# Performance work log

Hardware: AMD Instinct MI355X
Metric: run time of the kernel (lower is better)

The kernel has to match this reference:

```python
import jax, jax.numpy as jnp
import numpy as np

B, M, IN, H = 4096, 16, 512, 512


def _linear_params(key, out_dim, in_dim):
    kw, kb = jax.random.split(key)
    s = 1.0 / np.sqrt(in_dim)
    W = jax.random.uniform(kw, (out_dim, in_dim), jnp.float32, -s, s)
    b = jax.random.uniform(kb, (out_dim,), jnp.float32, -s, s)
    return W, b


def setup_inputs() -> dict:
    key = jax.random.key(0)
    ks = jax.random.split(key, 15)
    inp = {
        "input": jax.random.normal(ks[0], (B, IN), jnp.float32),
        "h0": jax.random.normal(ks[1], (B, H), jnp.float32),
        "c0": jax.random.normal(ks[2], (B, H), jnp.float32),
        "all_c_b_e_w": jax.random.normal(ks[3], (B, M, H), jnp.float32),
        "all_num_word": jax.random.randint(ks[4], (B,), 0, M + 1, jnp.int32),
    }
    names = ["ii", "hi", "if_", "hf", "ig", "hg", "io", "ho", "lx", "lc"]
    in_dims = [IN, H, IN, H, IN, H, IN, H, IN, H]
    for n, d, k in zip(names, in_dims, ks[5:15]):
        W, b = _linear_params(k, H, d)
        inp["W_" + n] = W
        inp["b_" + n] = b
    return inp


def _lin(x, W, b):
    return x @ W.T + b


def reference(input, h0, c0, all_c_b_e_w, all_num_word,
              W_ii, b_ii, W_hi, b_hi, W_if_, b_if_, W_hf, b_hf,
              W_ig, b_ig, W_hg, b_hg, W_io, b_io, W_ho, b_ho,
              W_lx, b_lx, W_lc, b_lc):
    i = jax.nn.sigmoid(_lin(input, W_ii, b_ii) + _lin(h0, W_hi, b_hi))   # [B,H]
    f = jax.nn.sigmoid(_lin(input, W_if_, b_if_) + _lin(h0, W_hf, b_hf))  # computed but unused, as in original
    g = jnp.tanh(_lin(input, W_ig, b_ig) + _lin(h0, W_hg, b_hg))         # [B,H]
    o = jax.nn.sigmoid(_lin(input, W_io, b_io) + _lin(h0, W_ho, b_ho))   # [B,H]

    # lattice word-cell gates, vectorized over the ragged word dim with a mask
    lx = _lin(input, W_lx, b_lx)                 # [B,H]
    lc = _lin(all_c_b_e_w, W_lc, b_lc)           # [B,M,H]
    i_b = jax.nn.sigmoid(lx[:, None, :] + lc)    # [B,M,H]
    mask = (jnp.arange(M)[None, :] < all_num_word[:, None])  # [B,M]
    exp_b = jnp.exp(i_b) * mask[:, :, None].astype(i_b.dtype)  # [B,M,H]
    exp_i = jnp.exp(i)                                         # [B,H]
    denom = exp_i + jnp.sum(exp_b, axis=1)                     # [B,H]
    c_words = jnp.sum((exp_b / denom[:, None, :]) * all_c_b_e_w, axis=1)
    c_lat = c_words + (exp_i / denom) * g
    c = jnp.where((all_num_word > 0)[:, None], c_lat, g)       # num_word==0 -> c=g
    h1 = o * jnp.tanh(c)
    return (h1, c)
```

## Files before the change

kernel.cpp:

```cpp
#include <hip/hip_runtime.h>
#include <stdint.h>


typedef __attribute__((ext_vector_type(8))) short short8;
typedef __attribute__((ext_vector_type(4))) float f32x4;
typedef __attribute__((ext_vector_type(4))) unsigned short us4;

__device__ __forceinline__ unsigned short f2bf(float f) {
  union { float f; unsigned u; } v; v.f = f;
  return (unsigned short)((v.u + 0x7fffu + ((v.u >> 16) & 1u)) >> 16);
}
__device__ __forceinline__ float bf2f(unsigned short u) {
  return __uint_as_float((unsigned)u << 16);
}
__device__ __forceinline__ float sigmoidf_(float x) {
  return 1.f / (1.f + __expf(-x));
}
__device__ __forceinline__ float fast_tanh(float x) {
  float e = __expf(-2.f * fmaxf(x, -30.f));
  return (1.f - e) / (1.f + e);
}

__global__ void k_cvt_xh(const float* __restrict__ x, const float* __restrict__ h,
                         unsigned short* __restrict__ out) {
  int t = blockIdx.x * blockDim.x + threadIdx.x;
  int b = t >> 8;
  int col = (t & 255) * 4;
  const float* src = (col < 512) ? (x + (size_t)b * 512 + col)
                                 : (h + (size_t)b * 512 + (col - 512));
  f32x4 v = *(const f32x4*)src;
  us4 o;
  o[0] = f2bf(v[0]); o[1] = f2bf(v[1]); o[2] = f2bf(v[2]); o[3] = f2bf(v[3]);
  *(us4*)(out + (size_t)t * 4) = o;
}

__global__ void k_cvt_w(const float* __restrict__ Wii, const float* __restrict__ Wig,
                        const float* __restrict__ Wio, const float* __restrict__ Wlx,
                        const float* __restrict__ Whi, const float* __restrict__ Whg,
                        const float* __restrict__ Who, unsigned short* __restrict__ out) {
  int t = blockIdx.x * blockDim.x + threadIdx.x;
  int row = t >> 8;
  int col = (t & 255) * 4;
  int sec = row >> 9, r = row & 511;
  us4 o;
  if (col < 512) {
    const float* W = sec == 0 ? Wii : sec == 1 ? Wig : sec == 2 ? Wio : Wlx;
    f32x4 v = *(const f32x4*)(W + (size_t)r * 512 + col);
    o[0] = f2bf(v[0]); o[1] = f2bf(v[1]); o[2] = f2bf(v[2]); o[3] = f2bf(v[3]);
  } else if (sec < 3) {
    const float* W = sec == 0 ? Whi : sec == 1 ? Whg : Who;
    f32x4 v = *(const f32x4*)(W + (size_t)r * 512 + (col - 512));
    o[0] = f2bf(v[0]); o[1] = f2bf(v[1]); o[2] = f2bf(v[2]); o[3] = f2bf(v[3]);
  } else {
    o[0] = 0; o[1] = 0; o[2] = 0; o[3] = 0;
  }
  *(us4*)(out + (size_t)t * 4) = o;
}

__global__ void k_cvt_wlc(const float* __restrict__ src, unsigned short* __restrict__ out) {
  int t = blockIdx.x * blockDim.x + threadIdx.x;
  f32x4 v = *(const f32x4*)(src + (size_t)t * 4);
  us4 o;
  o[0] = f2bf(v[0]); o[1] = f2bf(v[1]); o[2] = f2bf(v[2]); o[3] = f2bf(v[3]);
  *(us4*)(out + (size_t)t * 4) = o;
}

__global__ __launch_bounds__(256) void k_gemm0(
    const unsigned short* __restrict__ A, const unsigned short* __restrict__ Bm,
    unsigned short* __restrict__ C, int Ndim, int Kdim, int nbx) {
  __shared__ unsigned short As[2][128 * 64];
  __shared__ unsigned short Bs[2][128 * 64];
  const int tid = threadIdx.x;
  const int lane = tid & 63, wid = tid >> 6;
  const int wr = wid >> 1, wc = wid & 1;
  const int l15 = lane & 15, lhi = lane >> 4;

  const int chunk = gridDim.x >> 3;
  const int bid = (blockIdx.x & 7) * chunk + (blockIdx.x >> 3);
  const int brow = bid / nbx, bcol = bid % nbx;
  const int m0 = brow * 128, n0 = bcol * 128;

  f32x4 acc[4][4];
#pragma unroll
  for (int i = 0; i < 4; ++i)
#pragma unroll
    for (int j = 0; j < 4; ++j) acc[i][j] = (f32x4){0.f, 0.f, 0.f, 0.f};

  const int cb0 = wid * 64;
  auto stage = [&](int buf, int k0) {
#pragma unroll
    for (int q = 0; q < 4; ++q) {
      const int cb = q * 256 + cb0;
      const int chunkid = cb + lane;
      const int row = chunkid >> 3, slot = chunkid & 7;
      const int kk = k0 + ((slot ^ (row & 7)) << 3);
      __builtin_amdgcn_global_load_lds(
          (const __attribute__((address_space(1))) unsigned int*)(A + (size_t)(m0 + row) * Kdim + kk),
          (__attribute__((address_space(3))) unsigned int*)(As[buf] + cb * 8), 16, 0, 0);
      __builtin_amdgcn_global_load_lds(
          (const __attribute__((address_space(1))) unsigned int*)(Bm + (size_t)(n0 + row) * Kdim + kk),
          (__attribute__((address_space(3))) unsigned int*)(Bs[buf] + cb * 8), 16, 0, 0);
    }
  };

  const int nt = Kdim >> 6;
  stage(0, 0);
  __syncthreads();

  const int swz = (lane & 7) << 4;
  for (int t = 0; t < nt; ++t) {
    const int cur = t & 1;
    if (t + 1 < nt) stage(cur ^ 1, (t + 1) << 6);
    const char* Ab = (const char*)As[cur];
    const char* Bb = (const char*)Bs[cur];
#pragma unroll
    for (int s = 0; s < 2; ++s) {
      short8 av[4], bv[4];
#pragma unroll
      for (int mi = 0; mi < 4; ++mi) {
        const int row = wr * 64 + mi * 16 + l15;
        av[mi] = *(const short8*)(Ab + row * 128 + ((s * 64 + lhi * 16) ^ swz));
      }
#pragma unroll
      for (int ni = 0; ni < 4; ++ni) {
        const int row = wc * 64 + ni * 16 + l15;
        bv[ni] = *(const short8*)(Bb + row * 128 + ((s * 64 + lhi * 16) ^ swz));
      }
#pragma unroll
      for (int mi = 0; mi < 4; ++mi)
#pragma unroll
        for (int ni = 0; ni < 4; ++ni)
          acc[mi][ni] = __builtin_amdgcn_mfma_f32_16x16x32_bf16(av[mi], bv[ni], acc[mi][ni], 0, 0, 0);
    }
    __syncthreads();
  }

#pragma unroll
  for (int mi = 0; mi < 4; ++mi) {
    const int gr = m0 + wr * 64 + mi * 16 + lhi * 4;
#pragma unroll
    for (int ni = 0; ni < 4; ++ni) {
      const int gc = n0 + wc * 64 + ni * 16 + l15;
#pragma unroll
      for (int j = 0; j < 4; ++j)
        C[(size_t)(gr + j) * Ndim + gc] = f2bf(acc[mi][ni][j]);
    }
  }
}

__global__ __launch_bounds__(512) void k_latg(
    const float* __restrict__ Af,
    const unsigned short* __restrict__ Bm,
    unsigned short* __restrict__ lcb) {
  __shared__ unsigned short As[2][256 * 64];
  __shared__ unsigned short Bs[2][256 * 64];
  const int tid = threadIdx.x;
  const int lane = tid & 63, wid = tid >> 6;
  const int wrow = wid >> 2, wcol = wid & 3;
  const int l15 = lane & 15, lhi = lane >> 4;

  const int chunk = gridDim.x >> 3;
  const int bid = (blockIdx.x & 7) * chunk + (blockIdx.x >> 3);
  const int brow = bid >> 1, bcol = bid & 1;
  const int m0 = brow * 256, n0 = bcol * 256;

  f32x4 acc[8][4];
#pragma unroll
  for (int i = 0; i < 8; ++i)
#pragma unroll
    for (int j = 0; j < 4; ++j) acc[i][j] = (f32x4){0.f, 0.f, 0.f, 0.f};

  f32x4 ar[4][2];
  auto loadA = [&](int k0) {
#pragma unroll
    for (int q = 0; q < 4; ++q) {
      const int c = q * 512 + tid;
      const int row = c >> 3, slot = c & 7;
      const float* p = Af + (size_t)(m0 + row) * 512 + k0 + slot * 8;
      ar[q][0] = *(const f32x4*)p;
      ar[q][1] = *(const f32x4*)(p + 4);
    }
  };
  auto writeA = [&](int buf) {
#pragma unroll
    for (int q = 0; q < 4; ++q) {
      const int c = q * 512 + tid;
      const int row = c >> 3, slot = c & 7;
      short8 v;
      v[0] = (short)f2bf(ar[q][0][0]); v[1] = (short)f2bf(ar[q][0][1]);
      v[2] = (short)f2bf(ar[q][0][2]); v[3] = (short)f2bf(ar[q][0][3]);
      v[4] = (short)f2bf(ar[q][1][0]); v[5] = (short)f2bf(ar[q][1][1]);
      v[6] = (short)f2bf(ar[q][1][2]); v[7] = (short)f2bf(ar[q][1][3]);
      *(short8*)((char*)As[buf] + row * 128 + ((slot ^ (row & 7)) << 4)) = v;
    }
  };
  auto stageB = [&](int buf, int k0) {
#pragma unroll
    for (int q = 0; q < 4; ++q) {
      const int cb = q * 512 + wid * 64;
      const int c = cb + lane;
      const int row = c >> 3, slot = c & 7;
      const int kk = k0 + ((slot ^ (row & 7)) << 3);
      __builtin_amdgcn_global_load_lds(
          (const __attribute__((address_space(1))) unsigned int*)(Bm + (size_t)(n0 + row) * 512 + kk),
          (__attribute__((address_space(3))) unsigned int*)(Bs[buf] + cb * 8), 16, 0, 0);
    }
  };

  loadA(0);
  stageB(0, 0);
  writeA(0);
  __syncthreads();

  for (int t = 0; t < 8; ++t) {
    const int cur = t & 1;
    if (t < 7) {
      loadA((t + 1) << 6);
      stageB(cur ^ 1, (t + 1) << 6);
    }
    const char* Ab = (const char*)As[cur];
    const char* Bb = (const char*)Bs[cur];
#pragma unroll
    for (int s = 0; s < 2; ++s) {
      short8 av[8], bv[4];
#pragma unroll
      for (int mi = 0; mi < 8; ++mi) {
        const int row = wrow * 128 + mi * 16 + l15;
        av[mi] = *(const short8*)(Ab + row * 128 + ((s * 64 + lhi * 16) ^ ((row & 7) << 4)));
      }
#pragma unroll
      for (int ni = 0; ni < 4; ++ni) {
        const int row = wcol * 64 + ni * 16 + l15;
        bv[ni] = *(const short8*)(Bb + row * 128 + ((s * 64 + lhi * 16) ^ ((row & 7) << 4)));
      }
#pragma unroll
      for (int mi = 0; mi < 8; ++mi)
#pragma unroll
        for (int ni = 0; ni < 4; ++ni)
          acc[mi][ni] = __builtin_amdgcn_mfma_f32_16x16x32_bf16(av[mi], bv[ni], acc[mi][ni], 0, 0, 0);
    }
    if (t < 7) writeA(cur ^ 1);
    __syncthreads();
  }

#pragma unroll
  for (int mi = 0; mi < 8; ++mi) {
    const int gr = m0 + wrow * 128 + mi * 16 + lhi * 4;
#pragma unroll
    for (int ni = 0; ni < 4; ++ni) {
      const int gc = n0 + wcol * 64 + ni * 16 + l15;
#pragma unroll
      for (int j = 0; j < 4; ++j)
        lcb[(size_t)(gr + j) * 512 + gc] = f2bf(acc[mi][ni][j]);
    }
  }
}

__global__ __launch_bounds__(512) void k_epi(
    const unsigned short* __restrict__ lc,
    const float* __restrict__ all_c,
    const unsigned short* __restrict__ C1u,
    const int* __restrict__ num_word,
    const float* __restrict__ b_ii, const float* __restrict__ b_hi,
    const float* __restrict__ b_ig, const float* __restrict__ b_hg,
    const float* __restrict__ b_io, const float* __restrict__ b_ho,
    const float* __restrict__ b_lx, const float* __restrict__ b_lc,
    float* __restrict__ outH, float* __restrict__ outC) {
  const int b = blockIdx.x;
  const int hc = threadIdx.x;
  const int nw = num_word[b];
  const size_t base = (size_t)b * 2048;

  const float pre = bf2f(C1u[base + 1536 + hc]) + b_lx[hc] + b_lc[hc];
  const unsigned short* lcp = lc + ((size_t)b * 16) * 512 + hc;
  const float* wp = all_c + ((size_t)b * 16) * 512 + hc;

  float se = 0.f, sew = 0.f;
#pragma unroll 4
  for (int m = 0; m < nw; ++m) {
    const float ib = sigmoidf_(pre + bf2f(lcp[(size_t)m * 512]));
    const float e = __expf(ib);
    se += e;
    sew += e * wp[(size_t)m * 512];
  }

  const float ig = sigmoidf_(bf2f(C1u[base + hc]) + b_ii[hc] + b_hi[hc]);
  const float g  = fast_tanh(bf2f(C1u[base + 512 + hc]) + b_ig[hc] + b_hg[hc]);
  const float og = sigmoidf_(bf2f(C1u[base + 1024 + hc]) + b_io[hc] + b_ho[hc]);
  const float ei = __expf(ig);
  const float denom = ei + se;
  const float cc = (sew + ei * g) / denom;
  outH[(size_t)b * 512 + hc] = og * fast_tanh(cc);
  outC[(size_t)b * 512 + hc] = cc;
}

extern "C" void kernel_launch(void* const* d_in, const int* in_sizes, int n_in,
                              void* d_out, int out_size, void* d_ws, size_t ws_size,
                              hipStream_t stream) {
  const float* input    = (const float*)d_in[0];
  const float* h0       = (const float*)d_in[1];
  const float* all_c    = (const float*)d_in[3];
  const int*   num_word = (const int*)d_in[4];
  const float* W_ii = (const float*)d_in[5];  const float* b_ii = (const float*)d_in[6];
  const float* W_hi = (const float*)d_in[7];  const float* b_hi = (const float*)d_in[8];
  const float* W_ig = (const float*)d_in[13]; const float* b_ig = (const float*)d_in[14];
  const float* W_hg = (const float*)d_in[15]; const float* b_hg = (const float*)d_in[16];
  const float* W_io = (const float*)d_in[17]; const float* b_io = (const float*)d_in[18];
  const float* W_ho = (const float*)d_in[19]; const float* b_ho = (const float*)d_in[20];
  const float* W_lx = (const float*)d_in[21]; const float* b_lx = (const float*)d_in[22];
  const float* W_lc = (const float*)d_in[23]; const float* b_lc = (const float*)d_in[24];

  char* ws = (char*)d_ws;
  unsigned short* XH   = (unsigned short*)(ws);
  unsigned short* Wcat = (unsigned short*)(ws + 8388608);
  unsigned short* Wlc  = (unsigned short*)(ws + 12582912);
  unsigned short* C1u  = (unsigned short*)(ws + 13107200);
  unsigned short* lc   = (unsigned short*)(ws + 29884416);

  float* outH = (float*)d_out;
  float* outC = outH + (size_t)4096 * 512;

  k_cvt_xh<<<4096, 256, 0, stream>>>(input, h0, XH);
  k_cvt_w<<<2048, 256, 0, stream>>>(W_ii, W_ig, W_io, W_lx, W_hi, W_hg, W_ho, Wcat);
  k_cvt_wlc<<<256, 256, 0, stream>>>(W_lc, Wlc);

  k_gemm0<<<512, 256, 0, stream>>>(XH, Wcat, C1u, 2048, 1024, 16);

  k_latg<<<512, 512, 0, stream>>>(all_c, Wlc, lc);

  k_epi<<<4096, 512, 0, stream>>>(lc, all_c, C1u, num_word,
      b_ii, b_hi, b_ig, b_hg, b_io, b_ho, b_lx, b_lc, outH, outC);
}
```

Baseline: 123.3 us.

## Restructure lattice GEMM to LDS-free register-direct loads with smaller row tiles

The lattice-cell GEMM drops its double-buffered shared-memory staging. Each block now computes 64 full rows across all 512 columns, and each wave loads its A and B MFMA fragments straight from global memory into registers, prefetching one k-step ahead in software. The grid doubles to 1024 blocks, and the A conversion uses the library bf16 round-to-nearest-even intrinsic. This removes LDS traffic, barriers and the 256x256 tile's large register footprint. In exchange, all eight waves re-read the same A rows and every block reads the whole B matrix, so the load falls on L1/L2 reuse and uncoalesced fragment-sized global loads.

```diff
diff --git a/kernel.cpp b/kernel.cpp
--- a/kernel.cpp
+++ b/kernel.cpp
@@ -1,4 +1,5 @@
 #include <hip/hip_runtime.h>
+#include <hip/hip_bf16.h>
 #include <stdint.h>
 
 
@@ -9,6 +10,10 @@
 __device__ __forceinline__ unsigned short f2bf(float f) {
   union { float f; unsigned u; } v; v.f = f;
   return (unsigned short)((v.u + 0x7fffu + ((v.u >> 16) & 1u)) >> 16);
+}
+__device__ __forceinline__ unsigned short f2bf_rte(float f) {
+  __hip_bfloat16 h = __float2bfloat16(f);
+  return *reinterpret_cast<unsigned short*>(&h);
 }
 __device__ __forceinline__ float bf2f(unsigned short u) {
   return __uint_as_float((unsigned)u << 16);
@@ -152,103 +157,81 @@
     const float* __restrict__ Af,
     const unsigned short* __restrict__ Bm,
     unsigned short* __restrict__ lcb) {
-  __shared__ unsigned short As[2][256 * 64];
-  __shared__ unsigned short Bs[2][256 * 64];
   const int tid = threadIdx.x;
   const int lane = tid & 63, wid = tid >> 6;
-  const int wrow = wid >> 2, wcol = wid & 3;
   const int l15 = lane & 15, lhi = lane >> 4;
 
   const int chunk = gridDim.x >> 3;
   const int bid = (blockIdx.x & 7) * chunk + (blockIdx.x >> 3);
-  const int brow = bid >> 1, bcol = bid & 1;
-  const int m0 = brow * 256, n0 = bcol * 256;
-
-  f32x4 acc[8][4];
-#pragma unroll
-  for (int i = 0; i < 8; ++i)
+  const int m0 = bid * 64;
+
+  f32x4 acc[4][4];
+#pragma unroll
+  for (int i = 0; i < 4; ++i)
 #pragma unroll
     for (int j = 0; j < 4; ++j) acc[i][j] = (f32x4){0.f, 0.f, 0.f, 0.f};
 
-  f32x4 ar[4][2];
-  auto loadA = [&](int k0) {
-#pragma unroll
-    for (int q = 0; q < 4; ++q) {
-      const int c = q * 512 + tid;
-      const int row = c >> 3, slot = c & 7;
-      const float* p = Af + (size_t)(m0 + row) * 512 + k0 + slot * 8;
-      ar[q][0] = *(const f32x4*)p;
-      ar[q][1] = *(const f32x4*)(p + 4);
-    }
-  };
-  auto writeA = [&](int buf) {
-#pragma unroll
-    for (int q = 0; q < 4; ++q) {
-      const int c = q * 512 + tid;
-      const int row = c >> 3, slot = c & 7;
-      short8 v;
-      v[0] = (short)f2bf(ar[q][0][0]); v[1] = (short)f2bf(ar[q][0][1]);
-      v[2] = (short)f2bf(ar[q][0][2]); v[3] = (short)f2bf(ar[q][0][3]);
-      v[4] = (short)f2bf(ar[q][1][0]); v[5] = (short)f2bf(ar[q][1][1]);
-      v[6] = (short)f2bf(ar[q][1][2]); v[7] = (short)f2bf(ar[q][1][3]);
-      *(short8*)((char*)As[buf] + row * 128 + ((slot ^ (row & 7)) << 4)) = v;
-    }
-  };
-  auto stageB = [&](int buf, int k0) {
-#pragma unroll
-    for (int q = 0; q < 4; ++q) {
-      const int cb = q * 512 + wid * 64;
-      const int c = cb + lane;
-      const int row = c >> 3, slot = c & 7;
-      const int kk = k0 + ((slot ^ (row & 7)) << 3);
-      __builtin_amdgcn_global_load_lds(
-          (const __attribute__((address_space(1))) unsigned int*)(Bm + (size_t)(n0 + row) * 512 + kk),
-          (__attribute__((address_space(3))) unsigned int*)(Bs[buf] + cb * 8), 16, 0, 0);
-    }
-  };
-
-  loadA(0);
-  stageB(0, 0);
-  writeA(0);
-  __syncthreads();
-
-  for (int t = 0; t < 8; ++t) {
-    const int cur = t & 1;
-    if (t < 7) {
-      loadA((t + 1) << 6);
-      stageB(cur ^ 1, (t + 1) << 6);
-    }
-    const char* Ab = (const char*)As[cur];
-    const char* Bb = (const char*)Bs[cur];
-#pragma unroll
-    for (int s = 0; s < 2; ++s) {
-      short8 av[8], bv[4];
-#pragma unroll
-      for (int mi = 0; mi < 8; ++mi) {
-        const int row = wrow * 128 + mi * 16 + l15;
-        av[mi] = *(const short8*)(Ab + row * 128 + ((s * 64 + lhi * 16) ^ ((row & 7) << 4)));
-      }
-#pragma unroll
-      for (int ni = 0; ni < 4; ++ni) {
-        const int row = wcol * 64 + ni * 16 + l15;
-        bv[ni] = *(const short8*)(Bb + row * 128 + ((s * 64 + lhi * 16) ^ ((row & 7) << 4)));
-      }
-#pragma unroll
-      for (int mi = 0; mi < 8; ++mi)
-#pragma unroll
-        for (int ni = 0; ni < 4; ++ni)
-          acc[mi][ni] = __builtin_amdgcn_mfma_f32_16x16x32_bf16(av[mi], bv[ni], acc[mi][ni], 0, 0, 0);
-    }
-    if (t < 7) writeA(cur ^ 1);
-    __syncthreads();
-  }
-
-#pragma unroll
-  for (int mi = 0; mi < 8; ++mi) {
-    const int gr = m0 + wrow * 128 + mi * 16 + lhi * 4;
+  const float* aptr = Af + (size_t)(m0 + l15) * 512 + lhi * 8;
+  const unsigned short* bptr = Bm + (size_t)(wid * 64 + l15) * 512 + lhi * 8;
+
+  f32x4 arA[4][2], arB[4][2];
+  short8 bvA[4], bvB[4];
+
+#define LDA(dst, t)                                                         \
+  {                                                                         \
+    _Pragma("unroll")                                                       \
+    for (int mi = 0; mi < 4; ++mi) {                                        \
+      const float* p = aptr + mi * 8192 + (t) * 32;                         \
+      dst[mi][0] = *(const f32x4*)p;                                        \
+      dst[mi][1] = *(const f32x4*)(p + 4);                                  \
+    }                                                                       \
+  }
+#define LDB(dst, t)                                                         \
+  {                                                                         \
+    _Pragma("unroll")                                                       \
+    for (int ni = 0; ni < 4; ++ni)                                          \
+      dst[ni] = *(const short8*)(bptr + ni * 8192 + (t) * 32);              \
+  }
+#define STEP(ar, bv)                                                        \
+  {                                                                         \
+    short8 av[4];                                                           \
+    _Pragma("unroll")                                                       \
+    for (int mi = 0; mi < 4; ++mi) {                                        \
+      _Pragma("unroll")                                                     \
+      for (int e = 0; e < 8; ++e)                                           \
+        av[mi][e] = (short)f2bf_rte(ar[mi][e >> 2][e & 3]);                 \
+    }                                                                       \
+    _Pragma("unroll")                                                       \
+    for (int mi = 0; mi < 4; ++mi)                                          \
+      _Pragma("unroll")                                                     \
+      for (int ni = 0; ni < 4; ++ni)                                        \
+        acc[mi][ni] = __builtin_amdgcn_mfma_f32_16x16x32_bf16(              \
+            av[mi], bv[ni], acc[mi][ni], 0, 0, 0);                          \
+  }
+
+  LDA(arA, 0);
+  LDB(bvA, 0);
+#pragma unroll
+  for (int t = 0; t < 16; t += 2) {
+    LDA(arB, t + 1);
+    LDB(bvB, t + 1);
+    STEP(arA, bvA);
+    if (t + 2 < 16) {
+      LDA(arA, t + 2);
+      LDB(bvA, t + 2);
+    }
+    STEP(arB, bvB);
+  }
+#undef LDA
+#undef LDB
+#undef STEP
+
+#pragma unroll
+  for (int mi = 0; mi < 4; ++mi) {
+    const int gr = m0 + mi * 16 + lhi * 4;
 #pragma unroll
     for (int ni = 0; ni < 4; ++ni) {
-      const int gc = n0 + wcol * 64 + ni * 16 + l15;
+      const int gc = wid * 64 + ni * 16 + l15;
 #pragma unroll
       for (int j = 0; j < 4; ++j)
         lcb[(size_t)(gr + j) * 512 + gc] = f2bf(acc[mi][ni][j]);
@@ -326,7 +309,7 @@
 
   k_gemm0<<<512, 256, 0, stream>>>(XH, Wcat, C1u, 2048, 1024, 16);
 
-  k_latg<<<512, 512, 0, stream>>>(all_c, Wlc, lc);
+  k_latg<<<1024, 512, 0, stream>>>(all_c, Wlc, lc);
 
   k_epi<<<4096, 512, 0, stream>>>(lc, all_c, C1u, num_word,
       b_ii, b_hi, b_ig, b_hg, b_io, b_ho, b_lx, b_lc, outH, outC);
```

After: 243.6 us. +97.6%, slower.
